# Kernel tuning notes

Hardware: AMD Instinct MI355X
Metric: run time of the kernel (lower is better)

The kernel has to match this reference:

```python
import jax, jax.numpy as jnp
import numpy as np

B, T, C = 8, 2048, 1024
H = 4 * C
N_LAYER, LAYER_ID = 12, 2
K_CLAMP = 60.0
LN_EPS = 1e-5


def _ln(x, g, b):
    m = jnp.mean(x, axis=-1, keepdims=True)
    v = jnp.var(x, axis=-1, keepdims=True)
    return (x - m) * jax.lax.rsqrt(v + LN_EPS) * g + b


def _mix(x, time_mix, combined_mix):
    # x: (B,T,C). Causal shift (zeros at t=0), anti-causal shift (zeros at t=T-1).
    c = x.shape[-1]
    xm1 = jnp.pad(x[:, :-1], ((0, 0), (1, 0), (0, 0)))
    xp1 = jnp.pad(x[:, 1:], ((0, 0), (0, 1), (0, 0)))
    xc = jnp.concatenate([xm1[..., :c // 2], xp1[..., c // 2:]], axis=-1)
    return x * time_mix + xm1 * (1.0 - time_mix) + xc * combined_mix


def _wkv(time_decay, time_first, k, v):
    # RWKV WKV exponential-decay linear recurrence (the custom CUDA kernel).
    # k, v: (B,T,C); k > 0 (already clamped+exp'd).
    # y_t = (a_t + exp(u)*k_t*v_t) / (b_t + exp(u)*k_t)
    # a_{t+1} = exp(-exp(w))*a_t + k_t*v_t ; b likewise with v=1.
    ed = jnp.exp(-jnp.exp(time_decay))  # per-step channel decay, (C,)
    eu = jnp.exp(time_first)            # current-token bonus, (C,)

    def step(carry, kv_t):
        a, b = carry
        kt, vt = kv_t
        y = (a + eu * kt * vt) / (b + eu * kt)
        return (ed * a + kt * vt, ed * b + kt), y

    kT = jnp.swapaxes(k, 0, 1)  # (T,B,C)
    vT = jnp.swapaxes(v, 0, 1)
    z = jnp.zeros_like(kT[0])
    _, y = jax.lax.scan(step, (z, z), (kT, vT))
    return jnp.swapaxes(y, 0, 1)  # (B,T,C)


def _time_mix_block(x, time_mix, combined_mix, time_decay, time_first, Wk, Wv, Wr, Wo):
    xm = _mix(x, time_mix, combined_mix)
    k = jnp.exp(jnp.minimum(xm @ Wk.T, K_CLAMP))
    v = xm @ Wv.T
    r = xm @ Wr.T
    wkv = _wkv(time_decay, time_first, k, v)
    return (jax.nn.sigmoid(r) * wkv) @ Wo.T


def _channel_mix_block(x, time_mix, combined_mix, Fk, Fv, Fr):
    xm = _mix(x, time_mix, combined_mix)
    k = jnp.square(jax.nn.relu(xm @ Fk.T))
    kv = k @ Fv.T
    return jax.nn.sigmoid(xm @ Fr.T) * kv


def setup_inputs():
    key = jax.random.key(0)
    ks = jax.random.split(key, 9)
    s = 0.02
    x = jax.random.normal(ks[0], (B, T, C), jnp.float32)
    # time_decay init per the module (f1/f2 interpolation over layers)
    h = np.arange(C, dtype=np.float64)
    frac = (LAYER_ID - 1) / (N_LAYER - 2)
    f1 = 3.0 + frac * (1.2 - 3.0)
    f2 = 0.65 + frac * (0.4 - 0.65)
    decay_speed = np.power(f2, h / (C - 1) * 7.0) * f1
    tm = jnp.concatenate([jnp.zeros(C // 2), jnp.ones(C // 2)]).reshape(1, 1, C).astype(jnp.float32)
    return dict(
        x=x,
        ln1_g=jnp.ones((C,), jnp.float32), ln1_b=jnp.zeros((C,), jnp.float32),
        ln2_g=jnp.ones((C,), jnp.float32), ln2_b=jnp.zeros((C,), jnp.float32),
        att_time_mix=tm,
        att_combined_mix=jnp.full((1, 1, C), 0.01, jnp.float32),
        time_decay=jnp.asarray(np.log(decay_speed), jnp.float32),
        time_first=jnp.full((C,), float(np.log(0.3)), jnp.float32),
        Wk=jax.random.normal(ks[1], (C, C), jnp.float32) * s,
        Wv=jax.random.normal(ks[2], (C, C), jnp.float32) * s,
        Wr=jax.random.normal(ks[3], (C, C), jnp.float32) * s,
        Wo=jax.random.normal(ks[4], (C, C), jnp.float32) * s,
        ffn_time_mix=tm,
        ffn_combined_mix=jnp.full((1, 1, C), 0.01, jnp.float32),
        Fk=jax.random.normal(ks[5], (H, C), jnp.float32) * s,
        Fv=jax.random.normal(ks[6], (C, H), jnp.float32) * s,
        Fr=jax.random.normal(ks[7], (C, C), jnp.float32) * s,
    )


def reference(x, ln1_g, ln1_b, ln2_g, ln2_b, att_time_mix, att_combined_mix,
              time_decay, time_first, Wk, Wv, Wr, Wo,
              ffn_time_mix, ffn_combined_mix, Fk, Fv, Fr):
    x = _ln(x, ln1_g, ln1_b)
    x = x + _time_mix_block(x, att_time_mix, att_combined_mix, time_decay, time_first, Wk, Wv, Wr, Wo)
    x = _ln(x, ln2_g, ln2_b)
    x = x + _channel_mix_block(x, ffn_time_mix, ffn_combined_mix, Fk, Fv, Fr)
    return x
```

## Files before the change

### kernel.cpp

```cpp
#include <hip/hip_runtime.h>
#include <hip/hip_bf16.h>

typedef float f32x4 __attribute__((ext_vector_type(4)));
typedef __bf16 bf16x8 __attribute__((ext_vector_type(8)));
typedef __bf16 bf16x4 __attribute__((ext_vector_type(4)));

#define DEVI static __device__ __forceinline__

DEVI void glds16(const void* g, void* l) {
  __builtin_amdgcn_global_load_lds((__attribute__((address_space(1))) void*)g,
                                   (__attribute__((address_space(3))) void*)l, 16, 0, 0);
}

DEVI f32x4 load4(const float* p) { return *(const f32x4*)p; }
DEVI f32x4 load4(const __bf16* p) {
  bf16x4 v = *(const bf16x4*)p;
  f32x4 o = { (float)v[0], (float)v[1], (float)v[2], (float)v[3] };
  return o;
}
DEVI void store4(float* p, f32x4 v) { *(f32x4*)p = v; }
DEVI void store4(__bf16* p, f32x4 v) {
  bf16x4 o = { (__bf16)v[0], (__bf16)v[1], (__bf16)v[2], (__bf16)v[3] };
  *(bf16x4*)p = o;
}

__global__ void cvt_bf16(const float* __restrict__ in, __bf16* __restrict__ out, int n4) {
  int i = blockIdx.x * 256 + threadIdx.x;
  if (i < n4) {
    f32x4 v = *(const f32x4*)(in + (size_t)i * 4);
    store4(out + (size_t)i * 4, v);
  }
}

template <typename TIN, typename TOUT>
__global__ __launch_bounds__(256) void ln_kernel(const TIN* __restrict__ x,
    const float* __restrict__ gw, const float* __restrict__ bw,
    TOUT* __restrict__ out) {
  const size_t row = blockIdx.x;
  f32x4 v = load4(x + row * 1024 + threadIdx.x * 4);
  float s = v[0] + v[1] + v[2] + v[3];
  float q = v[0]*v[0] + v[1]*v[1] + v[2]*v[2] + v[3]*v[3];
#pragma unroll
  for (int o = 32; o > 0; o >>= 1) { s += __shfl_down(s, o); q += __shfl_down(q, o); }
  __shared__ float ss[4], qq[4];
  const int w = threadIdx.x >> 6, l = threadIdx.x & 63;
  if (l == 0) { ss[w] = s; qq[w] = q; }
  __syncthreads();
  s = ss[0] + ss[1] + ss[2] + ss[3];
  q = qq[0] + qq[1] + qq[2] + qq[3];
  const float mean = s * (1.0f / 1024.0f);
  const float var = q * (1.0f / 1024.0f) - mean * mean;
  const float rstd = rsqrtf(var + 1e-5f);
  f32x4 g4 = *(const f32x4*)(gw + threadIdx.x * 4);
  f32x4 b4 = *(const f32x4*)(bw + threadIdx.x * 4);
  f32x4 o;
#pragma unroll
  for (int j = 0; j < 4; ++j) o[j] = (v[j] - mean) * rstd * g4[j] + b4[j];
  store4(out + row * 1024 + threadIdx.x * 4, o);
}

template <typename TIN>
__global__ __launch_bounds__(256) void mix_kernel(const TIN* __restrict__ x,
    const float* __restrict__ tm, const float* __restrict__ cm,
    __bf16* __restrict__ out) {
  const int idx = blockIdx.x * 256 + threadIdx.x;
  const int t = (idx >> 8) & 2047;
  const int c = (idx & 255) * 4;
  const size_t base = ((size_t)(idx >> 8) << 10) + c;
  f32x4 xv = load4(x + base);
  f32x4 xm1 = {0.f, 0.f, 0.f, 0.f}, xp1 = {0.f, 0.f, 0.f, 0.f};
  if (t > 0)    xm1 = load4(x + base - 1024);
  if (t < 2047) xp1 = load4(x + base + 1024);
  f32x4 tm4 = *(const f32x4*)(tm + c);
  f32x4 cm4 = *(const f32x4*)(cm + c);
  f32x4 xc = (c < 512) ? xm1 : xp1;
  f32x4 o;
#pragma unroll
  for (int j = 0; j < 4; ++j)
    o[j] = xv[j] * tm4[j] + xm1[j] * (1.0f - tm4[j]) + xc[j] * cm4[j];
  store4(out + base, o);
}

__global__ __launch_bounds__(256) void wkv_part(const __bf16* __restrict__ k,
    const __bf16* __restrict__ v, const float* __restrict__ td,
    float* __restrict__ scA, float* __restrict__ scB) {
  const int gid = blockIdx.x * 256 + threadIdx.x;
  const int c = gid & 1023;
  const int j = (gid >> 10) & 31;
  const int b = gid >> 15;
  const float ed = expf(-expf(td[c]));
  float A = 0.f, Bv = 0.f;
  size_t off = ((size_t)(b * 2048 + j * 64) << 10) + c;
#pragma unroll 4
  for (int i = 0; i < 64; ++i, off += 1024) {
    const float kt = (float)k[off];
    const float kv = kt * (float)v[off];
    A = ed * A + kv;
    Bv = ed * Bv + kt;
  }
  scA[gid] = A;
  scB[gid] = Bv;
}

__global__ __launch_bounds__(256) void wkv_scan(const float* __restrict__ td,
    float* __restrict__ scA, float* __restrict__ scB) {
  const int gid = blockIdx.x * 256 + threadIdx.x;
  const int c = gid & 1023;
  const int b = gid >> 10;
  const float edL = expf(-expf(td[c]) * 64.0f);
  float a = 0.f, bb = 0.f;
  size_t off = ((size_t)b << 15) + c;
  for (int j = 0; j < 32; ++j, off += 1024) {
    const float Aj = scA[off], Bj = scB[off];
    scA[off] = a;
    scB[off] = bb;
    a = edL * a + Aj;
    bb = edL * bb + Bj;
  }
}

__global__ __launch_bounds__(256) void wkv_apply(const __bf16* __restrict__ k,
    const __bf16* __restrict__ v, const __bf16* __restrict__ sr,
    const float* __restrict__ td, const float* __restrict__ tf,
    const float* __restrict__ scA, const float* __restrict__ scB,
    __bf16* __restrict__ srw) {
  const int gid = blockIdx.x * 256 + threadIdx.x;
  const int c = gid & 1023;
  const int j = (gid >> 10) & 31;
  const int b = gid >> 15;
  const float ed = expf(-expf(td[c]));
  const float eu = expf(tf[c]);
  float a = scA[gid], bb = scB[gid];
  size_t off = ((size_t)(b * 2048 + j * 64) << 10) + c;
#pragma unroll 4
  for (int i = 0; i < 64; ++i, off += 1024) {
    const float kt = (float)k[off];
    const float vt = (float)v[off];
    const float kv = kt * vt;
    const float y = (a + eu * kv) / (bb + eu * kt);
    srw[off] = (__bf16)((float)sr[off] * y);
    a = ed * a + kv;
    bb = ed * bb + kt;
  }
}

enum { EPI_NONE = 0, EPI_EXP, EPI_SIG, EPI_RELU2, EPI_RESID, EPI_FINAL, EPI_KVR };

#define SBAR() { __builtin_amdgcn_s_barrier(); __builtin_amdgcn_sched_barrier(0); }
#define WAITL0() { asm volatile("s_waitcnt lgkmcnt(0)" ::: "memory"); __builtin_amdgcn_sched_barrier(0); }

template <int EPI>
__global__ __launch_bounds__(512, 2) void gemm256(
    const __bf16* __restrict__ A, const __bf16* __restrict__ W,
    void* outp, const void* res, const void* sig, const int N, const int K) {
  __shared__ __bf16 sA[4][8192];
  __shared__ __bf16 sB[4][8192];
  const int tid = threadIdx.x;
  const int w = tid >> 6, l = tid & 63;
  const int wm = w >> 2, wn = w & 3;

  const int nwg = gridDim.x * gridDim.y;
  int wg = blockIdx.y * gridDim.x + blockIdx.x;
  wg = (wg & 7) * (nwg >> 3) + (wg >> 3);
  const int m0 = (wg / gridDim.x) << 8;
  const int n0 = (wg % gridDim.x) << 8;

  const int cswz = (l & 3) ^ ((l >> 2) & 3) ^ (l >> 4);
  const int rst = w * 16 + (l >> 2);
  const size_t dA0 = (size_t)(m0 + rst) * K + cswz * 8;
  const size_t dA1 = dA0 + (size_t)128 * K;
  const size_t dB0 = (size_t)(n0 + rst) * K + cswz * 8;
  const size_t dB1 = dB0 + (size_t)128 * K;
  const int NT = K >> 5;

  auto stA = [&](int t) {
    const int s = t & 3;
    const size_t ko = (size_t)t << 5;
    glds16(A + dA0 + ko, &sA[s][w * 512]);
    glds16(A + dA1 + ko, &sA[s][(8 + w) * 512]);
  };
  auto stB = [&](int t) {
    const int s = t & 3;
    const size_t ko = (size_t)t << 5;
    glds16(W + dB0 + ko, &sB[s][w * 512]);
    glds16(W + dB1 + ko, &sB[s][(8 + w) * 512]);
  };

  const int fl = (l & 3) ^ ((l >> 2) & 3);
  const int coff = ((l >> 4) ^ fl) << 3;
  const int aoff = ((wm << 7) + (l & 15)) * 32 + coff;
  const int boff = ((wn << 6) + (l & 15)) * 32 + coff;

  f32x4 acc[8][4] = {};

  stA(0); stB(0); stA(1); stB(1); stA(2); stB(2);
  asm volatile("s_waitcnt vmcnt(8)" ::: "memory");
  __builtin_amdgcn_sched_barrier(0);
  SBAR();

  for (int kt = 0; kt < NT; ++kt) {
    const int slot = kt & 3;
    const __bf16* pa = &sA[slot][aoff];
    const __bf16* pb = &sB[slot][boff];
    bf16x8 bfr[4], afr[4];
#pragma unroll
    for (int i = 0; i < 4; ++i) bfr[i] = *(const bf16x8*)(pb + i * 512);
#pragma unroll
    for (int i = 0; i < 4; ++i) afr[i] = *(const bf16x8*)(pa + i * 512);
    if (kt + 3 < NT) stA(kt + 3);
    __builtin_amdgcn_sched_barrier(0);
    SBAR();
    WAITL0();
    __builtin_amdgcn_s_setprio(1);
#pragma unroll
    for (int mi = 0; mi < 4; ++mi)
#pragma unroll
      for (int ni = 0; ni < 4; ++ni)
        acc[mi][ni] = __builtin_amdgcn_mfma_f32_16x16x32_bf16(afr[mi], bfr[ni], acc[mi][ni], 0, 0, 0);
    __builtin_amdgcn_s_setprio(0);
    __builtin_amdgcn_sched_barrier(0);
    SBAR();
#pragma unroll
    for (int i = 0; i < 4; ++i) afr[i] = *(const bf16x8*)(pa + (4 + i) * 512);
    if (kt + 3 < NT) stB(kt + 3);
    __builtin_amdgcn_sched_barrier(0);
    SBAR();
    WAITL0();
    __builtin_amdgcn_s_setprio(1);
#pragma unroll
    for (int mi = 0; mi < 4; ++mi)
#pragma unroll
      for (int ni = 0; ni < 4; ++ni)
        acc[4 + mi][ni] = __builtin_amdgcn_mfma_f32_16x16x32_bf16(afr[mi], bfr[ni], acc[4 + mi][ni], 0, 0, 0);
    __builtin_amdgcn_s_setprio(0);
    const int rem = NT - 2 - kt;
    if (rem >= 2)      { asm volatile("s_waitcnt vmcnt(8)" ::: "memory"); }
    else if (rem == 1) { asm volatile("s_waitcnt vmcnt(4)" ::: "memory"); }
    else               { asm volatile("s_waitcnt vmcnt(0)" ::: "memory"); }
    __builtin_amdgcn_sched_barrier(0);
    SBAR();
  }

  const int rl = (l >> 4) << 2, cl = l & 15;
#pragma unroll
  for (int mi = 0; mi < 8; ++mi) {
#pragma unroll
    for (int ni = 0; ni < 4; ++ni) {
#pragma unroll
      for (int e = 0; e < 4; ++e) {
        const int r = m0 + (wm << 7) + mi * 16 + rl + e;
        const int cidx = n0 + (wn << 6) + ni * 16 + cl;
        const size_t idx = (size_t)r * N + cidx;
        const float vacc = acc[mi][ni][e];
        if constexpr (EPI == EPI_NONE) {
          ((__bf16*)outp)[idx] = (__bf16)vacc;
        } else if constexpr (EPI == EPI_EXP) {
          ((__bf16*)outp)[idx] = (__bf16)expf(fminf(vacc, 60.0f));
        } else if constexpr (EPI == EPI_SIG) {
          ((__bf16*)outp)[idx] = (__bf16)(1.0f / (1.0f + expf(-vacc)));
        } else if constexpr (EPI == EPI_RELU2) {
          const float rv = fmaxf(vacc, 0.0f);
          ((__bf16*)outp)[idx] = (__bf16)(rv * rv);
        } else if constexpr (EPI == EPI_RESID) {
          ((__bf16*)outp)[idx] = (__bf16)(vacc + (float)((const __bf16*)res)[idx]);
        } else if constexpr (EPI == EPI_FINAL) {
          ((float*)outp)[idx] = ((const float*)res)[idx] + (float)((const __bf16*)sig)[idx] * vacc;
        } else {
          const int sel = cidx >> 10;
          const size_t oidx = (size_t)r * 1024 + (cidx & 1023);
          if (sel == 0)      ((__bf16*)outp)[oidx] = (__bf16)expf(fminf(vacc, 60.0f));
          else if (sel == 1) ((__bf16*)const_cast<void*>(res))[oidx] = (__bf16)vacc;
          else               ((__bf16*)const_cast<void*>(sig))[oidx] = (__bf16)(1.0f / (1.0f + expf(-vacc)));
        }
      }
    }
  }
}

extern "C" void kernel_launch(void* const* d_in, const int* in_sizes, int n_in,
                              void* d_out, int out_size, void* d_ws, size_t ws_size,
                              hipStream_t stream) {
  (void)in_sizes; (void)n_in; (void)out_size;
  const float* x    = (const float*)d_in[0];
  const float* ln1g = (const float*)d_in[1];
  const float* ln1b = (const float*)d_in[2];
  const float* ln2g = (const float*)d_in[3];
  const float* ln2b = (const float*)d_in[4];
  const float* atm  = (const float*)d_in[5];
  const float* acm  = (const float*)d_in[6];
  const float* td   = (const float*)d_in[7];
  const float* tf   = (const float*)d_in[8];
  const float* Wk   = (const float*)d_in[9];
  const float* Wv   = (const float*)d_in[10];
  const float* Wr   = (const float*)d_in[11];
  const float* Wo   = (const float*)d_in[12];
  const float* ftm  = (const float*)d_in[13];
  const float* fcm  = (const float*)d_in[14];
  const float* Fk   = (const float*)d_in[15];
  const float* Fv   = (const float*)d_in[16];
  const float* Fr   = (const float*)d_in[17];

  constexpr size_t C = 1024, T = 2048, Bs = 8, H = 4096;
  constexpr size_t NT = Bs * T;
  constexpr size_t NTC = NT * C;
  constexpr size_t CC = C * C;
  constexpr size_t CH = C * H;

  char* p = (char*)d_ws;
  auto takeb = [&](size_t elems) { __bf16* q = (__bf16*)p; p += elems * 2; return q; };
  __bf16* wKVR = takeb(3 * CC);
  __bf16* wWo  = takeb(CC);
  __bf16* wFk  = takeb(CH);
  __bf16* wFv  = takeb(CH);
  __bf16* wFr  = takeb(CC);
  __bf16* Ab   = takeb(NTC);
  __bf16* Bb   = takeb(NTC);
  __bf16* Db   = takeb(NTC);
  float* scA = (float*)p; p += Bs * 32 * C * 4;
  float* scB = (float*)p; p += Bs * 32 * C * 4;
  __bf16* kk = (__bf16*)p;
  const size_t used = (size_t)(p - (char*)d_ws);
  const size_t kkcap = ws_size > used ? ws_size - used : 0;
  int chunks = 4;
  if (kkcap >= NT * H * 2)          chunks = 1;
  else if (kkcap >= NT * H)         chunks = 2;
  __bf16* Cb = kk;
  __bf16* sr  = (__bf16*)d_out;
  float*  x3  = (float*)d_out;

  auto cvt = [&](const float* src, size_t n, __bf16* dst) {
    const int n4 = (int)(n / 4);
    cvt_bf16<<<dim3((n4 + 255) / 256), dim3(256), 0, stream>>>(src, dst, n4);
  };
  cvt(Wk, CC, wKVR); cvt(Wv, CC, wKVR + CC); cvt(Wr, CC, wKVR + 2 * CC);
  cvt(Wo, CC, wWo); cvt(Fk, CH, wFk); cvt(Fv, CH, wFv); cvt(Fr, CC, wFr);

  const dim3 blk(256), blkG(512);

  ln_kernel<float, __bf16><<<dim3((unsigned)NT), blk, 0, stream>>>(x, ln1g, ln1b, Ab);
  mix_kernel<__bf16><<<dim3((unsigned)(NTC / 1024)), blk, 0, stream>>>(Ab, atm, acm, Bb);
  gemm256<EPI_KVR><<<dim3(12, 64), blkG, 0, stream>>>(Bb, wKVR, Cb, Db, sr, 3072, 1024);
  wkv_part<<<dim3(1024), blk, 0, stream>>>(Cb, Db, td, scA, scB);
  wkv_scan<<<dim3(32), blk, 0, stream>>>(td, scA, scB);
  wkv_apply<<<dim3(1024), blk, 0, stream>>>(Cb, Db, sr, td, tf, scA, scB, Bb);
  gemm256<EPI_RESID><<<dim3(4, 64), blkG, 0, stream>>>(Bb, wWo, Ab, Ab, nullptr, 1024, 1024);
  ln_kernel<__bf16, float><<<dim3((unsigned)NT), blk, 0, stream>>>(Ab, ln2g, ln2b, x3);
  mix_kernel<float><<<dim3((unsigned)(NTC / 1024)), blk, 0, stream>>>(x3, ftm, fcm, Db);
  gemm256<EPI_SIG><<<dim3(4, 64), blkG, 0, stream>>>(Db, wFr, Bb, nullptr, nullptr, 1024, 1024);
  const size_t Mc = NT / chunks;
  for (int ch = 0; ch < chunks; ++ch) {
    const size_t ro = (size_t)ch * Mc;
    gemm256<EPI_RELU2><<<dim3(16, (unsigned)(Mc / 256)), blkG, 0, stream>>>(
        Db + ro * C, wFk, kk, nullptr, nullptr, 4096, 1024);
    gemm256<EPI_FINAL><<<dim3(4, (unsigned)(Mc / 256)), blkG, 0, stream>>>(
        kk, wFv, (float*)d_out + ro * C, (const float*)d_out + ro * C,
        Bb + ro * C, 1024, 4096);
  }
}
```

Before: 783.3 us.

## Restructure GEMM into double-buffered BK=64 pipeline with four MFMA phases

The 256x256 bf16 GEMM moves from a 4-slot, BK=32 ring buffer to a 2-slot, BK=64 double buffer, with a new XOR-swizzled LDS layout. Each k-tile is split into four MFMA quadrants, and global-to-LDS staging for the next tile is interleaved between them with explicit vmcnt waits. The aim is fewer barriers per unit of K and better overlap of loads with MFMA work. In exchange the prefetch depth is shorter, since only one tile is in flight instead of three, and the LDS footprint stays the same.

```diff
diff --git a/kernel.cpp b/kernel.cpp
--- a/kernel.cpp
+++ b/kernel.cpp
@@ -148,13 +148,14 @@
 
 #define SBAR() { __builtin_amdgcn_s_barrier(); __builtin_amdgcn_sched_barrier(0); }
 #define WAITL0() { asm volatile("s_waitcnt lgkmcnt(0)" ::: "memory"); __builtin_amdgcn_sched_barrier(0); }
+#define VMW(n) { asm volatile("s_waitcnt vmcnt(" #n ")" ::: "memory"); __builtin_amdgcn_sched_barrier(0); }
 
 template <int EPI>
-__global__ __launch_bounds__(512, 2) void gemm256(
+__global__ __launch_bounds__(512, 2) void gemm8p(
     const __bf16* __restrict__ A, const __bf16* __restrict__ W,
     void* outp, const void* res, const void* sig, const int N, const int K) {
-  __shared__ __bf16 sA[4][8192];
-  __shared__ __bf16 sB[4][8192];
+  __shared__ __bf16 sA[2][16384];
+  __shared__ __bf16 sB[2][16384];
   const int tid = threadIdx.x;
   const int w = tid >> 6, l = tid & 63;
   const int wm = w >> 2, wn = w & 3;
@@ -165,80 +166,102 @@
   const int m0 = (wg / gridDim.x) << 8;
   const int n0 = (wg % gridDim.x) << 8;
 
-  const int cswz = (l & 3) ^ ((l >> 2) & 3) ^ (l >> 4);
-  const int rst = w * 16 + (l >> 2);
-  const size_t dA0 = (size_t)(m0 + rst) * K + cswz * 8;
-  const size_t dA1 = dA0 + (size_t)128 * K;
-  const size_t dB0 = (size_t)(n0 + rst) * K + cswz * 8;
-  const size_t dB1 = dB0 + (size_t)128 * K;
-  const int NT = K >> 5;
-
-  auto stA = [&](int t) {
-    const int s = t & 3;
-    const size_t ko = (size_t)t << 5;
-    glds16(A + dA0 + ko, &sA[s][w * 512]);
-    glds16(A + dA1 + ko, &sA[s][(8 + w) * 512]);
-  };
-  auto stB = [&](int t) {
-    const int s = t & 3;
-    const size_t ko = (size_t)t << 5;
-    glds16(W + dB0 + ko, &sB[s][w * 512]);
-    glds16(W + dB1 + ko, &sB[s][(8 + w) * 512]);
-  };
-
-  const int fl = (l & 3) ^ ((l >> 2) & 3);
-  const int coff = ((l >> 4) ^ fl) << 3;
-  const int aoff = ((wm << 7) + (l & 15)) * 32 + coff;
-  const int boff = ((wn << 6) + (l & 15)) * 32 + coff;
+  const int lr = l >> 3;
+  const int lc = (l & 7) ^ lr;
+  const size_t gA = (size_t)(m0 + w * 8 + lr) * K + lc * 8;
+  const size_t gB = (size_t)(n0 + wn * 64 + wm * 8 + lr) * K + lc * 8;
+  const int ldsA = w * 512;
+  const int ldsB = (wn * 64 + wm * 8) * 64;
+
+  const int NTK = K >> 6;
+
+#define STAGE_A(buf, kt, i) glds16(A + gA + (size_t)(i) * 64 * K + (size_t)(kt) * 64, &sA[buf][ldsA + (i) * 4096])
+#define STAGE_B(buf, kt, j) glds16(W + gB + (size_t)(j) * 16 * K + (size_t)(kt) * 64, &sB[buf][ldsB + (j) * 1024])
+
+  const int rA = (wm * 128 + (l & 15)) * 64;
+  const int rB = (wn * 64 + (l & 15)) * 64;
+  const int csw = l & 7;
+  const int k0 = l >> 4;
+#define LDA(buf, mi, kk) (*(const bf16x8*)&sA[buf][rA + (mi) * 1024 + ((((kk) * 4 + k0) ^ csw) << 3)])
+#define LDB(buf, ni, kk) (*(const bf16x8*)&sB[buf][rB + (ni) * 1024 + ((((kk) * 4 + k0) ^ csw) << 3)])
 
   f32x4 acc[8][4] = {};
-
-  stA(0); stB(0); stA(1); stB(1); stA(2); stB(2);
-  asm volatile("s_waitcnt vmcnt(8)" ::: "memory");
-  __builtin_amdgcn_sched_barrier(0);
-  SBAR();
-
-  for (int kt = 0; kt < NT; ++kt) {
-    const int slot = kt & 3;
-    const __bf16* pa = &sA[slot][aoff];
-    const __bf16* pb = &sB[slot][boff];
-    bf16x8 bfr[4], afr[4];
-#pragma unroll
-    for (int i = 0; i < 4; ++i) bfr[i] = *(const bf16x8*)(pb + i * 512);
-#pragma unroll
-    for (int i = 0; i < 4; ++i) afr[i] = *(const bf16x8*)(pa + i * 512);
-    if (kt + 3 < NT) stA(kt + 3);
-    __builtin_amdgcn_sched_barrier(0);
-    SBAR();
+  bf16x8 afr[8], b0[4], b1[4];
+
+  STAGE_B(0, 0, 0); STAGE_B(0, 0, 1); STAGE_A(0, 0, 0); STAGE_A(0, 0, 2);
+  STAGE_B(0, 0, 2); STAGE_B(0, 0, 3); STAGE_A(0, 0, 1); STAGE_A(0, 0, 3);
+
+  for (int kt = 0; kt < NTK; ++kt) {
+    const int buf = kt & 1, nb = buf ^ 1;
+    const bool st = (kt + 1 < NTK);
+    VMW(4); SBAR();
+#pragma unroll
+    for (int mi = 0; mi < 4; ++mi) {
+      afr[mi * 2 + 0] = LDA(buf, mi, 0);
+      afr[mi * 2 + 1] = LDA(buf, mi, 1);
+    }
+#pragma unroll
+    for (int ni = 0; ni < 2; ++ni) {
+      b0[ni * 2 + 0] = LDB(buf, ni, 0);
+      b0[ni * 2 + 1] = LDB(buf, ni, 1);
+    }
+    if (st) { STAGE_B(nb, kt + 1, 0); STAGE_B(nb, kt + 1, 1); }
     WAITL0();
     __builtin_amdgcn_s_setprio(1);
 #pragma unroll
     for (int mi = 0; mi < 4; ++mi)
 #pragma unroll
-      for (int ni = 0; ni < 4; ++ni)
-        acc[mi][ni] = __builtin_amdgcn_mfma_f32_16x16x32_bf16(afr[mi], bfr[ni], acc[mi][ni], 0, 0, 0);
+      for (int ni = 0; ni < 2; ++ni)
+#pragma unroll
+        for (int kk = 0; kk < 2; ++kk)
+          acc[mi][ni] = __builtin_amdgcn_mfma_f32_16x16x32_bf16(afr[mi*2+kk], b0[ni*2+kk], acc[mi][ni], 0, 0, 0);
     __builtin_amdgcn_s_setprio(0);
-    __builtin_amdgcn_sched_barrier(0);
+    if (st) { VMW(4); } else { VMW(2); }
     SBAR();
 #pragma unroll
-    for (int i = 0; i < 4; ++i) afr[i] = *(const bf16x8*)(pa + (4 + i) * 512);
-    if (kt + 3 < NT) stB(kt + 3);
-    __builtin_amdgcn_sched_barrier(0);
-    SBAR();
+    for (int ni = 0; ni < 2; ++ni) {
+      b1[ni * 2 + 0] = LDB(buf, ni + 2, 0);
+      b1[ni * 2 + 1] = LDB(buf, ni + 2, 1);
+    }
+    if (st) { STAGE_A(nb, kt + 1, 0); STAGE_A(nb, kt + 1, 2); }
     WAITL0();
     __builtin_amdgcn_s_setprio(1);
 #pragma unroll
     for (int mi = 0; mi < 4; ++mi)
 #pragma unroll
-      for (int ni = 0; ni < 4; ++ni)
-        acc[4 + mi][ni] = __builtin_amdgcn_mfma_f32_16x16x32_bf16(afr[mi], bfr[ni], acc[4 + mi][ni], 0, 0, 0);
+      for (int ni = 0; ni < 2; ++ni)
+#pragma unroll
+        for (int kk = 0; kk < 2; ++kk)
+          acc[mi][ni + 2] = __builtin_amdgcn_mfma_f32_16x16x32_bf16(afr[mi*2+kk], b1[ni*2+kk], acc[mi][ni + 2], 0, 0, 0);
     __builtin_amdgcn_s_setprio(0);
-    const int rem = NT - 2 - kt;
-    if (rem >= 2)      { asm volatile("s_waitcnt vmcnt(8)" ::: "memory"); }
-    else if (rem == 1) { asm volatile("s_waitcnt vmcnt(4)" ::: "memory"); }
-    else               { asm volatile("s_waitcnt vmcnt(0)" ::: "memory"); }
-    __builtin_amdgcn_sched_barrier(0);
+    if (st) { VMW(4); } else { VMW(0); }
     SBAR();
+#pragma unroll
+    for (int mi = 0; mi < 4; ++mi) {
+      afr[mi * 2 + 0] = LDA(buf, mi + 4, 0);
+      afr[mi * 2 + 1] = LDA(buf, mi + 4, 1);
+    }
+    if (st) { STAGE_B(nb, kt + 1, 2); STAGE_B(nb, kt + 1, 3); }
+    WAITL0();
+    __builtin_amdgcn_s_setprio(1);
+#pragma unroll
+    for (int mi = 0; mi < 4; ++mi)
+#pragma unroll
+      for (int ni = 0; ni < 2; ++ni)
+#pragma unroll
+        for (int kk = 0; kk < 2; ++kk)
+          acc[mi + 4][ni] = __builtin_amdgcn_mfma_f32_16x16x32_bf16(afr[mi*2+kk], b0[ni*2+kk], acc[mi + 4][ni], 0, 0, 0);
+    __builtin_amdgcn_s_setprio(0);
+    if (st) { STAGE_A(nb, kt + 1, 1); STAGE_A(nb, kt + 1, 3); }
+    __builtin_amdgcn_s_setprio(1);
+#pragma unroll
+    for (int mi = 0; mi < 4; ++mi)
+#pragma unroll
+      for (int ni = 0; ni < 2; ++ni)
+#pragma unroll
+        for (int kk = 0; kk < 2; ++kk)
+          acc[mi + 4][ni + 2] = __builtin_amdgcn_mfma_f32_16x16x32_bf16(afr[mi*2+kk], b1[ni*2+kk], acc[mi + 4][ni + 2], 0, 0, 0);
+    __builtin_amdgcn_s_setprio(0);
   }
 
   const int rl = (l >> 4) << 2, cl = l & 15;
@@ -339,20 +362,20 @@
 
   ln_kernel<float, __bf16><<<dim3((unsigned)NT), blk, 0, stream>>>(x, ln1g, ln1b, Ab);
   mix_kernel<__bf16><<<dim3((unsigned)(NTC / 1024)), blk, 0, stream>>>(Ab, atm, acm, Bb);
-  gemm256<EPI_KVR><<<dim3(12, 64), blkG, 0, stream>>>(Bb, wKVR, Cb, Db, sr, 3072, 1024);
+  gemm8p<EPI_KVR><<<dim3(12, 64), blkG, 0, stream>>>(Bb, wKVR, Cb, Db, sr, 3072, 1024);
   wkv_part<<<dim3(1024), blk, 0, stream>>>(Cb, Db, td, scA, scB);
   wkv_scan<<<dim3(32), blk, 0, stream>>>(td, scA, scB);
   wkv_apply<<<dim3(1024), blk, 0, stream>>>(Cb, Db, sr, td, tf, scA, scB, Bb);
-  gemm256<EPI_RESID><<<dim3(4, 64), blkG, 0, stream>>>(Bb, wWo, Ab, Ab, nullptr, 1024, 1024);
+  gemm8p<EPI_RESID><<<dim3(4, 64), blkG, 0, stream>>>(Bb, wWo, Ab, Ab, nullptr, 1024, 1024);
   ln_kernel<__bf16, float><<<dim3((unsigned)NT), blk, 0, stream>>>(Ab, ln2g, ln2b, x3);
   mix_kernel<float><<<dim3((unsigned)(NTC / 1024)), blk, 0, stream>>>(x3, ftm, fcm, Db);
-  gemm256<EPI_SIG><<<dim3(4, 64), blkG, 0, stream>>>(Db, wFr, Bb, nullptr, nullptr, 1024, 1024);
+  gemm8p<EPI_SIG><<<dim3(4, 64), blkG, 0, stream>>>(Db, wFr, Bb, nullptr, nullptr, 1024, 1024);
   const size_t Mc = NT / chunks;
   for (int ch = 0; ch < chunks; ++ch) {
     const size_t ro = (size_t)ch * Mc;
-    gemm256<EPI_RELU2><<<dim3(16, (unsigned)(Mc / 256)), blkG, 0, stream>>>(
+    gemm8p<EPI_RELU2><<<dim3(16, (unsigned)(Mc / 256)), blkG, 0, stream>>>(
         Db + ro * C, wFk, kk, nullptr, nullptr, 4096, 1024);
-    gemm256<EPI_FINAL><<<dim3(4, (unsigned)(Mc / 256)), blkG, 0, stream>>>(
+    gemm8p<EPI_FINAL><<<dim3(4, (unsigned)(Mc / 256)), blkG, 0, stream>>>(
         kk, wFv, (float*)d_out + ro * C, (const float*)d_out + ro * C,
         Bb + ro * C, 1024, 4096);
   }
```

Result: faster. 711.1 us (-9.2%).
